# Kernel optimization log

Hardware: AMD Instinct MI355X
Metric: run time of the kernel (lower is better)

Reference implementation:

```python
import jax, jax.numpy as jnp
import numpy as np

EPS = 1e-05  # norm_epsilon

def setup_inputs() -> dict:
    key = jax.random.key(0)
    ks = jax.random.split(key, 6)
    B, T, D, E, N, C = 16, 512, 256, 16, 8192, 1
    xs = jax.random.normal(ks[0], (B, T, D), jnp.float32)
    pad_mask = jnp.ones((B, T), dtype=bool)
    masked_masks = jax.random.randint(ks[1], (B, T), 0, 2) > 0
    ln_gamma = jnp.ones((D,), jnp.float32)
    ln_beta = jnp.zeros((D,), jnp.float32)
    # xavier_normal init for the (frozen) random projection
    projection = jax.random.normal(ks[2], (D, E), jnp.float32) * (2.0 / (D + E)) ** 0.5
    embeddings = jax.random.normal(ks[3], (C, E, N), jnp.float32)
    top_n_out = jax.random.normal(ks[4], (C, D, N), jnp.float32) * 0.02
    mask_emb = jax.random.normal(ks[5], (D,), jnp.float32) * 0.1
    return {"xs": xs, "pad_mask": pad_mask, "masked_masks": masked_masks,
            "ln_gamma": ln_gamma, "ln_beta": ln_beta, "projection": projection,
            "embeddings": embeddings, "top_n_out": top_n_out, "mask_emb": mask_emb}

def reference(xs, pad_mask, masked_masks, ln_gamma, ln_beta, projection, embeddings, top_n_out, mask_emb):
    B, T, D = xs.shape
    C = embeddings.shape[0]
    # ---- target path: layer norm -> random projection -> nearest codebook idx ----
    mu = jnp.mean(xs, -1, keepdims=True)
    var = jnp.mean((xs - mu) ** 2, -1, keepdims=True)
    h = (xs - mu) / jnp.sqrt(var + EPS) * ln_gamma + ln_beta
    proj = jnp.einsum('btd,de->bte', h, projection).reshape(B * T, -1)  # [BT,E]
    # pairwise squared distances: [C, BT, N]
    dist = (jnp.sum(proj ** 2, axis=1)[None, :, None]
            + jnp.sum(embeddings ** 2, axis=1)[:, None, :]
            - 2.0 * jnp.einsum('te,cen->ctn', proj, embeddings))
    target = jnp.argmin(dist, axis=-1).T.reshape(B, T, C)  # [B,T,C] int
    # ---- masked input -> encoder (identity stand-in) -> per-codebook logits ----
    masked_xs = jnp.where(masked_masks[..., None], mask_emb, xs)
    logits = jnp.einsum('btd,cdn->btcn', masked_xs, top_n_out)  # [B,T,C,N]
    logp = jax.nn.log_softmax(logits, axis=-1)
    ce = -jnp.take_along_axis(logp, target[..., None], axis=-1)[..., 0]  # [B,T,C]
    m = (pad_mask & masked_masks).astype(logits.dtype)  # [B,T]
    loss = jnp.sum(ce * m[..., None]) / (jnp.sum(m) * C)
    return loss
```

## Files before the change

### kernel.cpp

```cpp
#include <hip/hip_runtime.h>
#include <hip/hip_bf16.h>
#include <math.h>

#define BT   8192
#define DD   256
#define EE   16
#define NN   8192

typedef __attribute__((ext_vector_type(8))) short short8;
typedef __attribute__((ext_vector_type(4))) float f32x4;

__device__ __forceinline__ unsigned short f2bf(float x) {
  union { float f; unsigned int u; } c; c.f = x;
  unsigned int r = (c.u + 0x7FFFu + ((c.u >> 16) & 1u)) >> 16;
  return (unsigned short)r;
}
__device__ __forceinline__ unsigned int ordf(float d) {
  union { float f; unsigned int u; } c; c.f = d;
  return ((int)c.u < 0) ? ~c.u : (c.u | 0x80000000u);
}
__device__ __forceinline__ unsigned long long shflxor64(unsigned long long v, int m) {
  unsigned int lo = (unsigned int)v, hi = (unsigned int)(v >> 32);
  lo = __shfl_xor((int)lo, m);
  hi = __shfl_xor((int)hi, m);
  return ((unsigned long long)hi << 32) | lo;
}
__device__ __forceinline__ void gload_lds16(const void* g, void* l) {
  __builtin_amdgcn_global_load_lds((const __attribute__((address_space(1))) void*)g,
                                   (__attribute__((address_space(3))) void*)l, 16, 0, 0);
}

#define XT_LD 65
__global__ __launch_bounds__(256) void k_pre(const float* __restrict__ xs,
                                             const int* __restrict__ mm,
                                             const float* __restrict__ memb,
                                             const float* __restrict__ gamma,
                                             const float* __restrict__ beta,
                                             const float* __restrict__ P,
                                             const float* __restrict__ W,
                                             const float* __restrict__ emb,
                                             unsigned short* __restrict__ xmb,
                                             unsigned short* __restrict__ projb,
                                             unsigned short* __restrict__ Wt,
                                             unsigned short* __restrict__ embT,
                                             float* __restrict__ sqe,
                                             unsigned long long* __restrict__ keys,
                                             float* __restrict__ sumexp) {
  __shared__ __align__(16) float xt[32 * XT_LD * 4];
  __shared__ float stats[32][2];
  int bid = blockIdx.x;
  int tid = threadIdx.x;

  if (bid < 512) {
    int n0 = (bid & 127) * 64;
    int d0 = (bid >> 7) * 64;
    #pragma unroll
    for (int pass = 0; pass < 16; pass++) {
      int idx = pass * 256 + tid;
      int dd = idx >> 6, ln = idx & 63;
      xt[ln * 65 + dd] = W[(size_t)(d0 + dd) * NN + n0 + ln];
    }
    __syncthreads();
    #pragma unroll
    for (int pass = 0; pass < 2; pass++) {
      int g = pass * 256 + tid;
      int row = g >> 3, c8 = g & 7;
      short8 v;
      #pragma unroll
      for (int i = 0; i < 8; i++) v[i] = (short)f2bf(xt[row * 65 + c8 * 8 + i]);
      *(short8*)(Wt + (size_t)(n0 + row) * DD + d0 + c8 * 8) = v;
    }
    return;
  }
  if (bid < 544) {
    int n = (bid - 512) * 256 + tid;
    float e[EE];
    float sq = 0.f;
    #pragma unroll
    for (int k = 0; k < EE; k++) { e[k] = emb[k * NN + n]; sq += e[k] * e[k]; }
    short8 lo, hi;
    #pragma unroll
    for (int k = 0; k < 8; k++) { lo[k] = (short)f2bf(e[k]); hi[k] = (short)f2bf(e[k + 8]); }
    *(short8*)(embT + (size_t)n * EE)     = lo;
    *(short8*)(embT + (size_t)n * EE + 8) = hi;
    sqe[n] = sq;
    keys[n] = ~0ULL;
    return;
  }
  int pb = bid - 544;
  int t0 = pb * 32;
  int w = tid >> 6;
  int col4 = tid & 63;
  float4 mb4 = ((const float4*)memb)[col4];

  #pragma unroll
  for (int j = 0; j < 8; j++) {
    int k = tid + j * 256;
    int row = w + j * 4;
    float4 xv = ((const float4*)xs)[(size_t)pb * 2048 + k];
    int m = mm[t0 + row];
    float4 v = m ? mb4 : xv;
    ushort2 o01 = { f2bf(v.x), f2bf(v.y) };
    ushort2 o23 = { f2bf(v.z), f2bf(v.w) };
    ((ushort2*)(xmb + (size_t)(t0 + row) * DD + col4 * 4))[0] = o01;
    ((ushort2*)(xmb + (size_t)(t0 + row) * DD + col4 * 4))[1] = o23;
    *(float4*)&xt[(row * XT_LD + col4) * 4] = xv;
  }
  __syncthreads();
  {
    int t = tid >> 3, g = tid & 7;
    float s = 0.f, s2 = 0.f;
    #pragma unroll
    for (int i = 0; i < 8; i++) {
      float4 v = *(const float4*)&xt[(t * XT_LD + g * 8 + i) * 4];
      s  += v.x + v.y + v.z + v.w;
      s2 += v.x * v.x + v.y * v.y + v.z * v.z + v.w * v.w;
    }
    #pragma unroll
    for (int m = 1; m <= 4; m <<= 1) { s += __shfl_xor(s, m); s2 += __shfl_xor(s2, m); }
    if (g == 0) {
      float mu = s * (1.0f / DD);
      float var = s2 * (1.0f / DD) - mu * mu;
      stats[t][0] = mu;
      stats[t][1] = rsqrtf(var + 1e-5f);
    }
  }
  if (tid < 32) sumexp[t0 + tid] = 0.f;
  __syncthreads();
  {
    int t = tid >> 3, e0 = (tid & 7) * 2;
    float mu = stats[t][0], rstd = stats[t][1];
    float a0 = 0.f, a1 = 0.f;
    for (int d = 0; d < DD; d += 4) {
      float4 xv = *(const float4*)&xt[(t * XT_LD + (d >> 2)) * 4];
      float xd[4] = { xv.x, xv.y, xv.z, xv.w };
      #pragma unroll
      for (int dd = 0; dd < 4; dd++) {
        float h = (xd[dd] - mu) * rstd * gamma[d + dd] + beta[d + dd];
        a0 += h * P[(d + dd) * EE + e0];
        a1 += h * P[(d + dd) * EE + e0 + 1];
      }
    }
    ushort2 o = { f2bf(a0), f2bf(a1) };
    *(ushort2*)(projb + (size_t)(t0 + t) * EE + e0) = o;
  }
}

#define NS4 8
#define ASEG (NN / NS4)
__global__ __launch_bounds__(256) void k_argmin(const unsigned short* __restrict__ projb,
                                                const unsigned short* __restrict__ embT,
                                                const float* __restrict__ sqe,
                                                unsigned long long* __restrict__ keys) {
  int tid = threadIdx.x;
  int w = tid >> 6, lane = tid & 63;
  int q = lane >> 4, c = lane & 15;
  int tw = blockIdx.x * 64 + w * 16;
  int nseg = blockIdx.y * ASEG;

  short8 a = {0, 0, 0, 0, 0, 0, 0, 0};
  if (q < 2) a = *(const short8*)(projb + (size_t)(tw + c) * EE + q * 8);

  unsigned long long bk[4];
  #pragma unroll
  for (int r = 0; r < 4; r++) bk[r] = ~0ULL;

  #pragma unroll 2
  for (int it = 0; it < ASEG / 16; it++) {
    int n = nseg + it * 16 + c;
    short8 b = {0, 0, 0, 0, 0, 0, 0, 0};
    if (q < 2) b = *(const short8*)(embT + (size_t)n * EE + q * 8);
    float sq = sqe[n];
    f32x4 acc = (f32x4){0.f, 0.f, 0.f, 0.f};
    acc = __builtin_amdgcn_mfma_f32_16x16x32_bf16(a, b, acc, 0, 0, 0);
    #pragma unroll
    for (int r = 0; r < 4; r++) {
      float dist = sq - 2.f * acc[r];
      unsigned long long key = ((unsigned long long)ordf(dist) << 32) | (unsigned int)n;
      bk[r] = key < bk[r] ? key : bk[r];
    }
  }
  #pragma unroll
  for (int r = 0; r < 4; r++) {
    #pragma unroll
    for (int m = 1; m <= 8; m <<= 1) {
      unsigned long long o = shflxor64(bk[r], m);
      bk[r] = o < bk[r] ? o : bk[r];
    }
  }
  if (c == 0) {
    #pragma unroll
    for (int r = 0; r < 4; r++)
      atomicMin(&keys[tw + q * 4 + r], bk[r]);
  }
}

__global__ __launch_bounds__(512, 4) void k_ce5(const unsigned short* __restrict__ xmb,
                                                const unsigned short* __restrict__ Wt,
                                                const unsigned long long* __restrict__ keys,
                                                float* __restrict__ sumexp,
                                                float* __restrict__ ltar) {
  __shared__ __align__(16) unsigned short ldsA[3][256 * 32];
  __shared__ __align__(16) unsigned short ldsB[3][128 * 32];
  int tid = threadIdx.x;
  int lane = tid & 63;
  int w = tid >> 6;
  int q = lane >> 4, c = lane & 15;
  int wm = w >> 1, wn = w & 1;
  int t0 = blockIdx.x * 256;
  int n0 = blockIdx.y * 128;
  int sw = q ^ ((c >> 1) & 3);

  f32x4 acc[4][4];
  #pragma unroll
  for (int mi = 0; mi < 4; mi++)
    #pragma unroll
    for (int ni = 0; ni < 4; ni++) acc[mi][ni] = (f32x4){0.f, 0.f, 0.f, 0.f};

  #define STAGE(buf, itv) do {                                                  \
    int kk_ = (itv) * 32;                                                       \
    _Pragma("unroll")                                                           \
    for (int j = 0; j < 2; j++) {                                               \
      int g = j * 512 + tid;                                                    \
      int row = g >> 2;                                                         \
      int qg = (g & 3) ^ ((g >> 3) & 3);                                        \
      gload_lds16(xmb + (size_t)(t0 + row) * DD + kk_ + qg * 8,                 \
                  ldsA[buf] + g * 8);                                           \
    }                                                                           \
    {                                                                           \
      int g = tid;                                                              \
      int row = g >> 2;                                                         \
      int qg = (g & 3) ^ ((g >> 3) & 3);                                        \
      gload_lds16(Wt + (size_t)(n0 + row) * DD + kk_ + qg * 8,                  \
                  ldsB[buf] + g * 8);                                           \
    }                                                                           \
  } while (0)

  STAGE(0, 0);
  STAGE(1, 1);
  asm volatile("s_waitcnt vmcnt(3)" ::: "memory");
  __builtin_amdgcn_s_barrier();

  #pragma unroll
  for (int it = 0; it < 8; it++) {
    const int cur = it % 3;
    const int nxt = (it + 2) % 3;
    if (it + 2 < 8) {
      if (nxt == 0)      STAGE(0, it + 2);
      else if (nxt == 1) STAGE(1, it + 2);
      else               STAGE(2, it + 2);
    }

    short8 a[4];
    #pragma unroll
    for (int mi = 0; mi < 4; mi++)
      a[mi] = *(const short8*)(ldsA[cur] + (wm * 64 + mi * 16 + c) * 32 + sw * 8);
    #pragma unroll
    for (int ni = 0; ni < 4; ni++) {
      short8 b = *(const short8*)(ldsB[cur] + (wn * 64 + ni * 16 + c) * 32 + sw * 8);
      #pragma unroll
      for (int mi = 0; mi < 4; mi++)
        acc[mi][ni] = __builtin_amdgcn_mfma_f32_16x16x32_bf16(a[mi], b, acc[mi][ni], 0, 0, 0);
    }

    if (it < 6) {
      asm volatile("s_waitcnt vmcnt(3)" ::: "memory");
      __builtin_amdgcn_s_barrier();
    } else if (it == 6) {
      asm volatile("s_waitcnt vmcnt(0)" ::: "memory");
      __builtin_amdgcn_s_barrier();
    }
  }
  #undef STAGE

  #pragma unroll
  for (int mi = 0; mi < 4; mi++) {
    int rowb = t0 + wm * 64 + mi * 16 + q * 4;
    int tg[4];
    float rs[4];
    #pragma unroll
    for (int r = 0; r < 4; r++) {
      tg[r] = (int)(unsigned int)(keys[rowb + r] & 0xFFFFFFFFULL);
      rs[r] = 0.f;
    }
    #pragma unroll
    for (int ni = 0; ni < 4; ni++) {
      int col = n0 + wn * 64 + ni * 16 + c;
      #pragma unroll
      for (int r = 0; r < 4; r++) {
        float v = acc[mi][ni][r];
        if (col == tg[r])
          ltar[rowb + r] = v;
        rs[r] += __expf(v);
      }
    }
    #pragma unroll
    for (int r = 0; r < 4; r++) {
      float s = rs[r];
      s += __shfl_xor(s, 1);
      s += __shfl_xor(s, 2);
      s += __shfl_xor(s, 4);
      s += __shfl_xor(s, 8);
      if (c == 0)
        atomicAdd(&sumexp[rowb + r], s);
    }
  }
}

__global__ __launch_bounds__(1024) void k_final(const float* __restrict__ sumexp,
                                                const float* __restrict__ ltar,
                                                const int* __restrict__ padm,
                                                const int* __restrict__ mm,
                                                float* __restrict__ out) {
  int tid = threadIdx.x;
  float sum = 0.f, cnt = 0.f;
  for (int t = tid; t < BT; t += 1024) {
    float ce = __logf(sumexp[t]) - ltar[t];
    if (padm[t] && mm[t]) { sum += ce; cnt += 1.f; }
  }
  #pragma unroll
  for (int off = 32; off; off >>= 1) { sum += __shfl_down(sum, off); cnt += __shfl_down(cnt, off); }
  __shared__ float rs[16], rc[16];
  int wid = tid >> 6, lane = tid & 63;
  if (lane == 0) { rs[wid] = sum; rc[wid] = cnt; }
  __syncthreads();
  if (tid == 0) {
    float S = 0.f, Cn = 0.f;
    for (int i = 0; i < 16; i++) { S += rs[i]; Cn += rc[i]; }
    out[0] = S / Cn;
  }
}

extern "C" void kernel_launch(void* const* d_in, const int* in_sizes, int n_in,
                              void* d_out, int out_size, void* d_ws, size_t ws_size,
                              hipStream_t stream) {
  const float* xs    = (const float*)d_in[0];
  const int*   padm  = (const int*)d_in[1];
  const int*   mm    = (const int*)d_in[2];
  const float* gamma = (const float*)d_in[3];
  const float* beta  = (const float*)d_in[4];
  const float* P     = (const float*)d_in[5];
  const float* emb   = (const float*)d_in[6];
  const float* W     = (const float*)d_in[7];
  const float* memb  = (const float*)d_in[8];
  float* out = (float*)d_out;

  char* ws = (char*)d_ws;
  size_t off = 0;
  unsigned short* xmb   = (unsigned short*)(ws + off); off += (size_t)BT * DD * 2;
  unsigned short* Wtb   = (unsigned short*)(ws + off); off += (size_t)NN * DD * 2;
  unsigned short* embT  = (unsigned short*)(ws + off); off += (size_t)NN * EE * 2;
  unsigned short* projb = (unsigned short*)(ws + off); off += (size_t)BT * EE * 2;
  float* sqe            = (float*)(ws + off);          off += (size_t)NN * 4;
  unsigned long long* keys = (unsigned long long*)(ws + off); off += (size_t)BT * 8;
  float* sumexp         = (float*)(ws + off);          off += (size_t)BT * 4;
  float* ltar           = (float*)(ws + off);          off += (size_t)BT * 4;

  k_pre   <<<800, 256, 0, stream>>>(xs, mm, memb, gamma, beta, P, W, emb,
                                    xmb, projb, Wtb, embT, sqe, keys, sumexp);
  k_argmin<<<dim3(BT / 64, NS4), 256, 0, stream>>>(projb, embT, sqe, keys);
  k_ce5   <<<dim3(32, 64), 512, 0, stream>>>(xmb, Wtb, keys, sumexp, ltar);
  k_final <<<1, 1024, 0, stream>>>(sumexp, ltar, padm, mm, out);
}
```

Before: 176.0 us.

## Enlarge CE GEMM tile to 256x256 with K=64 stages; cache projection params in LDS

The cross-entropy GEMM kernel now uses 256x256 output tiles with a 64-wide K step, double buffering instead of triple buffering, and an XOR swizzle over 8 chunks. Each wave holds 8x4 MFMA accumulators, so operand reuse rises and the grid is halved. In exchange, LDS use and register pressure grow, and occupancy is lowered to 2 blocks per SM. Smaller changes stage the projection matrix, gamma and beta in LDS for the layer-norm projection, pre-halve the squared codebook norms to drop a multiply, and track the argmin with 32-bit compares instead of 64-bit keys.

```diff
diff --git a/kernel.cpp b/kernel.cpp
--- a/kernel.cpp
+++ b/kernel.cpp
@@ -48,6 +48,8 @@
                                              float* __restrict__ sumexp) {
   __shared__ __align__(16) float xt[32 * XT_LD * 4];
   __shared__ float stats[32][2];
+  __shared__ __align__(16) float Pl[DD * EE];
+  __shared__ __align__(16) float gl[DD], bl[DD];
   int bid = blockIdx.x;
   int tid = threadIdx.x;
 
@@ -83,7 +85,7 @@
     for (int k = 0; k < 8; k++) { lo[k] = (short)f2bf(e[k]); hi[k] = (short)f2bf(e[k + 8]); }
     *(short8*)(embT + (size_t)n * EE)     = lo;
     *(short8*)(embT + (size_t)n * EE + 8) = hi;
-    sqe[n] = sq;
+    sqe[n] = 0.5f * sq;
     keys[n] = ~0ULL;
     return;
   }
@@ -92,6 +94,14 @@
   int w = tid >> 6;
   int col4 = tid & 63;
   float4 mb4 = ((const float4*)memb)[col4];
+
+  #pragma unroll
+  for (int i = tid; i < DD * EE / 4; i += 256)
+    ((float4*)Pl)[i] = ((const float4*)P)[i];
+  if (tid < DD / 4) {
+    ((float4*)gl)[tid] = ((const float4*)gamma)[tid];
+    ((float4*)bl)[tid] = ((const float4*)beta)[tid];
+  }
 
   #pragma unroll
   for (int j = 0; j < 8; j++) {
@@ -136,9 +146,9 @@
       float xd[4] = { xv.x, xv.y, xv.z, xv.w };
       #pragma unroll
       for (int dd = 0; dd < 4; dd++) {
-        float h = (xd[dd] - mu) * rstd * gamma[d + dd] + beta[d + dd];
-        a0 += h * P[(d + dd) * EE + e0];
-        a1 += h * P[(d + dd) * EE + e0 + 1];
+        float h = (xd[dd] - mu) * rstd * gl[d + dd] + bl[d + dd];
+        a0 += h * Pl[(d + dd) * EE + e0];
+        a1 += h * Pl[(d + dd) * EE + e0 + 1];
       }
     }
     ushort2 o = { f2bf(a0), f2bf(a1) };
@@ -161,25 +171,29 @@
   short8 a = {0, 0, 0, 0, 0, 0, 0, 0};
   if (q < 2) a = *(const short8*)(projb + (size_t)(tw + c) * EE + q * 8);
 
-  unsigned long long bk[4];
-  #pragma unroll
-  for (int r = 0; r < 4; r++) bk[r] = ~0ULL;
+  unsigned int bo[4], bi[4];
+  #pragma unroll
+  for (int r = 0; r < 4; r++) { bo[r] = 0xFFFFFFFFu; bi[r] = 0u; }
 
   #pragma unroll 2
   for (int it = 0; it < ASEG / 16; it++) {
     int n = nseg + it * 16 + c;
     short8 b = {0, 0, 0, 0, 0, 0, 0, 0};
     if (q < 2) b = *(const short8*)(embT + (size_t)n * EE + q * 8);
-    float sq = sqe[n];
+    float sqh = sqe[n];
     f32x4 acc = (f32x4){0.f, 0.f, 0.f, 0.f};
     acc = __builtin_amdgcn_mfma_f32_16x16x32_bf16(a, b, acc, 0, 0, 0);
     #pragma unroll
     for (int r = 0; r < 4; r++) {
-      float dist = sq - 2.f * acc[r];
-      unsigned long long key = ((unsigned long long)ordf(dist) << 32) | (unsigned int)n;
-      bk[r] = key < bk[r] ? key : bk[r];
-    }
-  }
+      float dist = sqh - acc[r];
+      unsigned int u = ordf(dist);
+      if (u < bo[r]) { bo[r] = u; bi[r] = (unsigned int)n; }
+    }
+  }
+  unsigned long long bk[4];
+  #pragma unroll
+  for (int r = 0; r < 4; r++)
+    bk[r] = ((unsigned long long)bo[r] << 32) | bi[r];
   #pragma unroll
   for (int r = 0; r < 4; r++) {
     #pragma unroll
@@ -195,78 +209,74 @@
   }
 }
 
-__global__ __launch_bounds__(512, 4) void k_ce5(const unsigned short* __restrict__ xmb,
+__global__ __launch_bounds__(512, 2) void k_ce5(const unsigned short* __restrict__ xmb,
                                                 const unsigned short* __restrict__ Wt,
                                                 const unsigned long long* __restrict__ keys,
                                                 float* __restrict__ sumexp,
                                                 float* __restrict__ ltar) {
-  __shared__ __align__(16) unsigned short ldsA[3][256 * 32];
-  __shared__ __align__(16) unsigned short ldsB[3][128 * 32];
+  __shared__ __align__(16) unsigned short ldsA[2][256 * 64];
+  __shared__ __align__(16) unsigned short ldsB[2][256 * 64];
   int tid = threadIdx.x;
   int lane = tid & 63;
   int w = tid >> 6;
   int q = lane >> 4, c = lane & 15;
-  int wm = w >> 1, wn = w & 1;
+  int wm = w >> 2, wn = w & 3;
   int t0 = blockIdx.x * 256;
-  int n0 = blockIdx.y * 128;
-  int sw = q ^ ((c >> 1) & 3);
-
-  f32x4 acc[4][4];
-  #pragma unroll
-  for (int mi = 0; mi < 4; mi++)
+  int n0 = blockIdx.y * 256;
+
+  f32x4 acc[8][4];
+  #pragma unroll
+  for (int mi = 0; mi < 8; mi++)
     #pragma unroll
     for (int ni = 0; ni < 4; ni++) acc[mi][ni] = (f32x4){0.f, 0.f, 0.f, 0.f};
 
   #define STAGE(buf, itv) do {                                                  \
-    int kk_ = (itv) * 32;                                                       \
+    int kk0_ = (itv) * 64;                                                      \
     _Pragma("unroll")                                                           \
-    for (int j = 0; j < 2; j++) {                                               \
+    for (int j = 0; j < 4; j++) {                                               \
       int g = j * 512 + tid;                                                    \
-      int row = g >> 2;                                                         \
-      int qg = (g & 3) ^ ((g >> 3) & 3);                                        \
-      gload_lds16(xmb + (size_t)(t0 + row) * DD + kk_ + qg * 8,                 \
+      int row = g >> 3;                                                         \
+      int ch = (g & 7) ^ (row & 7);                                             \
+      gload_lds16(xmb + (size_t)(t0 + row) * DD + kk0_ + ch * 8,                \
                   ldsA[buf] + g * 8);                                           \
-    }                                                                           \
-    {                                                                           \
-      int g = tid;                                                              \
-      int row = g >> 2;                                                         \
-      int qg = (g & 3) ^ ((g >> 3) & 3);                                        \
-      gload_lds16(Wt + (size_t)(n0 + row) * DD + kk_ + qg * 8,                  \
+      gload_lds16(Wt + (size_t)(n0 + row) * DD + kk0_ + ch * 8,                 \
                   ldsB[buf] + g * 8);                                           \
     }                                                                           \
   } while (0)
 
   STAGE(0, 0);
-  STAGE(1, 1);
-  asm volatile("s_waitcnt vmcnt(3)" ::: "memory");
+  asm volatile("s_waitcnt vmcnt(0)" ::: "memory");
   __builtin_amdgcn_s_barrier();
 
   #pragma unroll
-  for (int it = 0; it < 8; it++) {
-    const int cur = it % 3;
-    const int nxt = (it + 2) % 3;
-    if (it + 2 < 8) {
-      if (nxt == 0)      STAGE(0, it + 2);
-      else if (nxt == 1) STAGE(1, it + 2);
-      else               STAGE(2, it + 2);
-    }
-
-    short8 a[4];
-    #pragma unroll
-    for (int mi = 0; mi < 4; mi++)
-      a[mi] = *(const short8*)(ldsA[cur] + (wm * 64 + mi * 16 + c) * 32 + sw * 8);
-    #pragma unroll
-    for (int ni = 0; ni < 4; ni++) {
-      short8 b = *(const short8*)(ldsB[cur] + (wn * 64 + ni * 16 + c) * 32 + sw * 8);
-      #pragma unroll
-      for (int mi = 0; mi < 4; mi++)
-        acc[mi][ni] = __builtin_amdgcn_mfma_f32_16x16x32_bf16(a[mi], b, acc[mi][ni], 0, 0, 0);
-    }
-
-    if (it < 6) {
-      asm volatile("s_waitcnt vmcnt(3)" ::: "memory");
-      __builtin_amdgcn_s_barrier();
-    } else if (it == 6) {
+  for (int it = 0; it < 4; it++) {
+    const int cur = it & 1;
+    if (it < 3) {
+      if (cur) STAGE(0, it + 1);
+      else     STAGE(1, it + 1);
+    }
+
+    #pragma unroll
+    for (int kk = 0; kk < 2; kk++) {
+      short8 a[8];
+      #pragma unroll
+      for (int mi = 0; mi < 8; mi++) {
+        int row = wm * 128 + mi * 16 + c;
+        int cs = (kk * 4 + q) ^ (row & 7);
+        a[mi] = *(const short8*)(ldsA[cur] + row * 64 + cs * 8);
+      }
+      #pragma unroll
+      for (int ni = 0; ni < 4; ni++) {
+        int col = wn * 64 + ni * 16 + c;
+        int cs = (kk * 4 + q) ^ (col & 7);
+        short8 b = *(const short8*)(ldsB[cur] + col * 64 + cs * 8);
+        #pragma unroll
+        for (int mi = 0; mi < 8; mi++)
+          acc[mi][ni] = __builtin_amdgcn_mfma_f32_16x16x32_bf16(a[mi], b, acc[mi][ni], 0, 0, 0);
+      }
+    }
+
+    if (it < 3) {
       asm volatile("s_waitcnt vmcnt(0)" ::: "memory");
       __builtin_amdgcn_s_barrier();
     }
@@ -274,8 +284,8 @@
   #undef STAGE
 
   #pragma unroll
-  for (int mi = 0; mi < 4; mi++) {
-    int rowb = t0 + wm * 64 + mi * 16 + q * 4;
+  for (int mi = 0; mi < 8; mi++) {
+    int rowb = t0 + wm * 128 + mi * 16 + q * 4;
     int tg[4];
     float rs[4];
     #pragma unroll
@@ -359,6 +369,6 @@
   k_pre   <<<800, 256, 0, stream>>>(xs, mm, memb, gamma, beta, P, W, emb,
                                     xmb, projb, Wtb, embT, sqe, keys, sumexp);
   k_argmin<<<dim3(BT / 64, NS4), 256, 0, stream>>>(projb, embT, sqe, keys);
-  k_ce5   <<<dim3(32, 64), 512, 0, stream>>>(xmb, Wtb, keys, sumexp, ltar);
+  k_ce5   <<<dim3(32, 32), 512, 0, stream>>>(xmb, Wtb, keys, sumexp, ltar);
   k_final <<<1, 1024, 0, stream>>>(sumexp, ltar, padm, mm, out);
 }
```

Result: slower. 204.9 us (+16.4%).
